# Optimization experiments

Measured on AMD Instinct MI355X. Metric: run time of the kernel, lower is better.

Reference implementation:

```python
import jax, jax.numpy as jnp
import numpy as np
from jax import lax

T, H, I, E, K = 1024, 1024, 512, 16, 4


def setup_inputs() -> dict:
    key = jax.random.key(0)
    k1, k2, k3, k4, k5 = jax.random.split(key, 5)
    hidden_states = jax.random.normal(k1, (T, H), dtype=jnp.float32)
    top_k_index = jax.random.randint(k2, (T, K), 0, E)
    top_k_weights = jax.random.uniform(k3, (T, K), dtype=jnp.float32)
    gate_up_proj = jax.random.normal(k4, (E, 2 * I, H), dtype=jnp.float32) * 0.02
    down_proj = jax.random.normal(k5, (E, H, I), dtype=jnp.float32) * 0.02
    return {
        "hidden_states": hidden_states,
        "top_k_index": top_k_index,
        "top_k_weights": top_k_weights,
        "gate_up_proj": gate_up_proj,
        "down_proj": down_proj,
    }


def reference(hidden_states, top_k_index, top_k_weights, gate_up_proj, down_proj):
    num_experts = gate_up_proj.shape[0]
    # combine[t, e] = sum_k top_k_weights[t, k] * [top_k_index[t, k] == e]
    # Expert output is linear in the routing weight, so summing weights over
    # duplicate (token, expert) hits matches the original index_add_ exactly.
    one_hot = jax.nn.one_hot(top_k_index, num_experts, dtype=hidden_states.dtype)  # [T, K, E]
    combine = jnp.einsum("tke,tk->te", one_hot, top_k_weights)  # [T, E]

    def expert_step(acc, xs):
        w_gu, w_d, c = xs  # [2I, H], [H, I], [T]
        gu = hidden_states @ w_gu.T          # [T, 2I]
        gate, up = jnp.split(gu, 2, axis=-1)
        h = jax.nn.silu(gate) * up            # [T, I]
        out = h @ w_d.T                       # [T, H]
        return acc + out * c[:, None], None

    final, _ = lax.scan(
        expert_step,
        jnp.zeros_like(hidden_states),
        (gate_up_proj, down_proj, combine.T),
    )
    return final
```

## Files before the change

kernel.cpp:

```cpp
#include <hip/hip_runtime.h>
#include <hip/hip_bf16.h>
#include <cstdint>
#include <cstddef>

#define T_TOK 1024
#define HDIM  1024
#define IDIM  512
#define NEXP  16
#define TOPK  4
#define CAP   1024

typedef __bf16 bf16;
typedef __attribute__((ext_vector_type(8))) __bf16 bf16x8;
typedef __attribute__((ext_vector_type(4))) __bf16 bf16x4;
typedef __attribute__((ext_vector_type(4))) float f32x4;

__device__ __forceinline__ void lds_load16(void* lds_dst, const void* g_src) {
  __builtin_amdgcn_global_load_lds(
      (__attribute__((address_space(1))) unsigned int*)(void*)(g_src),
      (__attribute__((address_space(3))) unsigned int*)(lds_dst),
      16, 0, 0);
}

__device__ __forceinline__ bf16x4 cvt4(float4 a) {
  bf16x4 o;
  o[0] = (bf16)a.x; o[1] = (bf16)a.y; o[2] = (bf16)a.z; o[3] = (bf16)a.w;
  return o;
}
__device__ __forceinline__ bf16x8 pack2(float4 a, float4 b) {
  bf16x8 o;
  o[0] = (bf16)a.x; o[1] = (bf16)a.y; o[2] = (bf16)a.z; o[3] = (bf16)a.w;
  o[4] = (bf16)b.x; o[5] = (bf16)b.y; o[6] = (bf16)b.z; o[7] = (bf16)b.w;
  return o;
}


#define CVT_BLOCKS (T_TOK * HDIM / 4 / 256)

__global__ void prep_kernel(const float* __restrict__ hid_f, bf16* __restrict__ hid_b,
                            const int* __restrict__ idx, const float* __restrict__ w,
                            int* __restrict__ etk, float* __restrict__ ew,
                            int* __restrict__ cntpad) {
  __shared__ int cnt;
  const int b = blockIdx.x;
  const int tid = threadIdx.x;
  if (b < CVT_BLOCKS) {
    int i = b * 256 + tid;
    float4 v = ((const float4*)hid_f)[i];
    ((bf16x4*)hid_b)[i] = cvt4(v);
    if (b == 0)
      ((bf16x4*)(hid_b + (size_t)T_TOK * HDIM))[tid] = cvt4(make_float4(0.f, 0.f, 0.f, 0.f));
    return;
  }
  const int e = b - CVT_BLOCKS;
  if (tid == 0) cnt = 0;
  __syncthreads();
  for (int j = tid; j < T_TOK * TOPK; j += blockDim.x) {
    if (idx[j] == e) {
      int slot = atomicAdd(&cnt, 1);
      if (slot < CAP) { etk[e * CAP + slot] = j; ew[e * CAP + slot] = w[j]; }
    }
  }
  __syncthreads();
  int c = cnt < CAP ? cnt : CAP;
  int p = (c + 63) & ~63;
  for (int j = c + tid; j < p; j += blockDim.x) {
    etk[e * CAP + j] = (T_TOK << 2);
    ew[e * CAP + j] = 0.f;
  }
  if (tid == 0) cntpad[e] = p;
}


__global__ __launch_bounds__(256, 3) void gemm1_kernel(
    const bf16* __restrict__ hid,
    const float* __restrict__ gup,
    const int* __restrict__ etk, const float* __restrict__ ew,
    const int* __restrict__ cntpad,
    bf16* __restrict__ hsc) {
  __shared__ __align__(16) bf16 As[2][64 * 128];
  __shared__ __align__(16) bf16 BgS[2][16 * 128];
  __shared__ __align__(16) bf16 BuS[2][16 * 128];
  const int e  = blockIdx.y;
  const int z  = blockIdx.z;
  const int trips = cntpad[e] >> 6;
  const int n0 = blockIdx.x * 16;
  const int ebase = e * CAP;
  const int tid = threadIdx.x, lane = tid & 63, wid = tid >> 6;
  const int wm = wid * 16;
  const int lcol = lane & 15, lquad = lane >> 4;
  const int arow0 = tid >> 4;
  const int swzA  = (((tid & 15) ^ (arow0 & 7)) * 8);
  const int br = tid >> 4;
  const int bc = (tid & 15) * 8;
  const int physB = ((tid & 15) ^ (br & 7)) * 8;
  const float* gBg = gup + (size_t)e * (2 * IDIM) * HDIM + (size_t)(n0 + br) * HDIM + bc;
  const float* gBu = gBg + (size_t)IDIM * HDIM;

  for (int m = z; m < trips; m += 2) {
    const int mb = ebase + m * 64;
    const bf16* gA[4];
#pragma unroll
    for (int i = 0; i < 4; ++i) {
      int t = etk[mb + arow0 + 16 * i] >> 2;
      gA[i] = hid + (size_t)t * HDIM + swzA;
    }
    float wgt[4];
#pragma unroll
    for (int rr = 0; rr < 4; ++rr) wgt[rr] = ew[mb + wm + lquad * 4 + rr];

    f32x4 aG = f32x4{0.f, 0.f, 0.f, 0.f};
    f32x4 aU = f32x4{0.f, 0.f, 0.f, 0.f};

#pragma unroll
    for (int i = 0; i < 4; ++i) lds_load16(&As[0][tid * 8 + i * 2048], gA[i]);
    {
      float4 g0 = *(const float4*)(gBg), g1 = *(const float4*)(gBg + 4);
      float4 u0 = *(const float4*)(gBu), u1 = *(const float4*)(gBu + 4);
      *(bf16x8*)&BgS[0][br * 128 + physB] = pack2(g0, g1);
      *(bf16x8*)&BuS[0][br * 128 + physB] = pack2(u0, u1);
    }
#pragma unroll 2
    for (int k = 0; k < 8; ++k) {
      const int cur = k & 1, nxt = cur ^ 1;
      __syncthreads();
      float4 g0, g1, u0, u1;
      if (k < 7) {
        const int ko = (k + 1) * 128;
#pragma unroll
        for (int i = 0; i < 4; ++i) lds_load16(&As[nxt][tid * 8 + i * 2048], gA[i] + ko);
        g0 = *(const float4*)(gBg + ko); g1 = *(const float4*)(gBg + ko + 4);
        u0 = *(const float4*)(gBu + ko); u1 = *(const float4*)(gBu + ko + 4);
      }
#pragma unroll
      for (int ks = 0; ks < 4; ++ks) {
        const int lch = ks * 4 + lquad;
        const int ar = wm + lcol;
        bf16x8 af = *(const bf16x8*)&As[cur][ar * 128 + ((lch ^ (ar & 7)) * 8)];
        bf16x8 bg = *(const bf16x8*)&BgS[cur][lcol * 128 + ((lch ^ (lcol & 7)) * 8)];
        bf16x8 bu = *(const bf16x8*)&BuS[cur][lcol * 128 + ((lch ^ (lcol & 7)) * 8)];
        aG = __builtin_amdgcn_mfma_f32_16x16x32_bf16(af, bg, aG, 0, 0, 0);
        aU = __builtin_amdgcn_mfma_f32_16x16x32_bf16(af, bu, aU, 0, 0, 0);
      }
      if (k < 7) {
        *(bf16x8*)&BgS[nxt][br * 128 + physB] = pack2(g0, g1);
        *(bf16x8*)&BuS[nxt][br * 128 + physB] = pack2(u0, u1);
      }
    }
#pragma unroll
    for (int rr = 0; rr < 4; ++rr) {
      const int erow = m * 64 + wm + lquad * 4 + rr;
      float g = aG[rr], u = aU[rr];
      float s = g / (1.f + __expf(-g));
      hsc[(size_t)(ebase + erow) * IDIM + n0 + lcol] = (bf16)(s * u * wgt[rr]);
    }
  }
}


__global__ __launch_bounds__(256, 3) void gemm2_kernel(
    const bf16* __restrict__ hsc,
    const float* __restrict__ down,
    const int* __restrict__ etk, const int* __restrict__ cntpad,
    float* __restrict__ slabs) {
  __shared__ __align__(16) bf16 As[2][64 * 128];
  __shared__ __align__(16) bf16 Bs[2][32 * 128];
  const int e  = blockIdx.y;
  const int z  = blockIdx.z;
  const int trips = cntpad[e] >> 6;
  const int n0 = blockIdx.x * 32;
  const int ebase = e * CAP;
  const int tid = threadIdx.x, lane = tid & 63, wid = tid >> 6;
  const int wm = wid * 16;
  const int lcol = lane & 15, lquad = lane >> 4;
  const int arow0 = tid >> 4;
  const int swzA  = (((tid & 15) ^ (arow0 & 7)) * 8);
  const int btr = tid >> 3;
  const int bc  = (tid & 7) * 16;
  const int cb0 = (tid & 7) * 2;
  const int physB0 = (cb0 ^ (btr & 7)) * 8;
  const int physB1 = ((cb0 + 1) ^ (btr & 7)) * 8;
  const float* gB = down + (size_t)e * HDIM * IDIM + (size_t)(n0 + btr) * IDIM + bc;

  for (int m = z; m < trips; m += 2) {
    const int mb = ebase + m * 64;
    const bf16* gA[4];
#pragma unroll
    for (int i = 0; i < 4; ++i)
      gA[i] = hsc + (size_t)(mb + arow0 + 16 * i) * IDIM + swzA;
    int tks[4];
#pragma unroll
    for (int rr = 0; rr < 4; ++rr) tks[rr] = etk[mb + wm + lquad * 4 + rr];

    f32x4 acc0 = f32x4{0.f, 0.f, 0.f, 0.f};
    f32x4 acc1 = f32x4{0.f, 0.f, 0.f, 0.f};

#pragma unroll
    for (int i = 0; i < 4; ++i) lds_load16(&As[0][tid * 8 + i * 2048], gA[i]);
    {
      float4 v0 = *(const float4*)(gB),     v1 = *(const float4*)(gB + 4);
      float4 v2 = *(const float4*)(gB + 8), v3 = *(const float4*)(gB + 12);
      *(bf16x8*)&Bs[0][btr * 128 + physB0] = pack2(v0, v1);
      *(bf16x8*)&Bs[0][btr * 128 + physB1] = pack2(v2, v3);
    }
#pragma unroll 2
    for (int k = 0; k < 4; ++k) {
      const int cur = k & 1, nxt = cur ^ 1;
      __syncthreads();
      float4 v0, v1, v2, v3;
      if (k < 3) {
        const int ko = (k + 1) * 128;
#pragma unroll
        for (int i = 0; i < 4; ++i) lds_load16(&As[nxt][tid * 8 + i * 2048], gA[i] + ko);
        v0 = *(const float4*)(gB + ko);     v1 = *(const float4*)(gB + ko + 4);
        v2 = *(const float4*)(gB + ko + 8); v3 = *(const float4*)(gB + ko + 12);
      }
#pragma unroll
      for (int ks = 0; ks < 4; ++ks) {
        const int lch = ks * 4 + lquad;
        const int ar = wm + lcol;
        bf16x8 af = *(const bf16x8*)&As[cur][ar * 128 + ((lch ^ (ar & 7)) * 8)];
        const int br0 = lcol, br1 = 16 + lcol;
        bf16x8 b0 = *(const bf16x8*)&Bs[cur][br0 * 128 + ((lch ^ (br0 & 7)) * 8)];
        bf16x8 b1 = *(const bf16x8*)&Bs[cur][br1 * 128 + ((lch ^ (br1 & 7)) * 8)];
        acc0 = __builtin_amdgcn_mfma_f32_16x16x32_bf16(af, b0, acc0, 0, 0, 0);
        acc1 = __builtin_amdgcn_mfma_f32_16x16x32_bf16(af, b1, acc1, 0, 0, 0);
      }
      if (k < 3) {
        *(bf16x8*)&Bs[nxt][btr * 128 + physB0] = pack2(v0, v1);
        *(bf16x8*)&Bs[nxt][btr * 128 + physB1] = pack2(v2, v3);
      }
    }
#pragma unroll
    for (int rr = 0; rr < 4; ++rr) {
      const int tok = tks[rr] >> 2, kslot = tks[rr] & 3;
      float* orow = slabs + ((size_t)kslot * (T_TOK + 1) + tok) * HDIM + n0;
      orow[lcol]      = acc0[rr];
      orow[16 + lcol] = acc1[rr];
    }
  }
}


__global__ void reduce_kernel(const float* __restrict__ slabs, float* __restrict__ out) {
  const size_t stride = (size_t)(T_TOK + 1) * HDIM;
  int i = blockIdx.x * blockDim.x + threadIdx.x;
  float4 a = ((const float4*)slabs)[i];
  float4 b = ((const float4*)(slabs + stride))[i];
  float4 c = ((const float4*)(slabs + 2 * stride))[i];
  float4 d = ((const float4*)(slabs + 3 * stride))[i];
  float4 o;
  o.x = a.x + b.x + c.x + d.x;
  o.y = a.y + b.y + c.y + d.y;
  o.z = a.z + b.z + c.z + d.z;
  o.w = a.w + b.w + c.w + d.w;
  ((float4*)out)[i] = o;
}


extern "C" void kernel_launch(void* const* d_in, const int* in_sizes, int n_in,
                              void* d_out, int out_size, void* d_ws, size_t ws_size,
                              hipStream_t stream) {
  const float* hid_f  = (const float*)d_in[0];
  const int*   idx    = (const int*)d_in[1];
  const float* tw     = (const float*)d_in[2];
  const float* gup_f  = (const float*)d_in[3];
  const float* down_f = (const float*)d_in[4];
  float* out = (float*)d_out;

  uint8_t* ws = (uint8_t*)d_ws;
  size_t off = 0;
  bf16* hid_b = (bf16*)(ws + off);   off += (size_t)(T_TOK + 1) * HDIM * 2;
  int*  etk   = (int*)(ws + off);    off += (size_t)NEXP * CAP * 4;
  float* ewt  = (float*)(ws + off);  off += (size_t)NEXP * CAP * 4;
  int* cntpad = (int*)(ws + off);    off += 256;
  bf16* hsc   = (bf16*)(ws + off);   off += (size_t)NEXP * CAP * IDIM * 2;
  float* slabs = (float*)(ws + off);

  prep_kernel<<<dim3(CVT_BLOCKS + NEXP), dim3(256), 0, stream>>>(
      hid_f, hid_b, idx, tw, etk, ewt, cntpad);
  gemm1_kernel<<<dim3(IDIM / 16, NEXP, 2), dim3(256), 0, stream>>>(
      hid_b, gup_f, etk, ewt, cntpad, hsc);
  gemm2_kernel<<<dim3(HDIM / 32, NEXP, 2), dim3(256), 0, stream>>>(
      hsc, down_f, etk, cntpad, slabs);
  reduce_kernel<<<dim3(T_TOK * HDIM / 4 / 256), dim3(256), 0, stream>>>(slabs, out);
}
```

Baseline: 207.4 us.

## Split LDS K-tiles into 64-wide halves and drop z-split of token tiles

Both expert GEMM kernels now store each 128-wide K tile as two 64-column sub-tiles with an 8-chunk XOR swizzle, which changes how global loads map to threads (coalescing per 128B row segment). The z-dimension split of token tiles is removed, so each block handles every M tile of its expert and column slice. The grid is halved and launch_bounds occupancy drops from 3 to 2. This cuts repeated fp32 weight loads per column slice and may improve global access patterns, but it lowers parallelism and occupancy.

```diff
diff --git a/kernel.cpp b/kernel.cpp
--- a/kernel.cpp
+++ b/kernel.cpp
@@ -72,39 +72,36 @@
 }
 
 
-__global__ __launch_bounds__(256, 3) void gemm1_kernel(
+__global__ __launch_bounds__(256, 2) void gemm1_kernel(
     const bf16* __restrict__ hid,
     const float* __restrict__ gup,
     const int* __restrict__ etk, const float* __restrict__ ew,
     const int* __restrict__ cntpad,
     bf16* __restrict__ hsc) {
-  __shared__ __align__(16) bf16 As[2][64 * 128];
-  __shared__ __align__(16) bf16 BgS[2][16 * 128];
-  __shared__ __align__(16) bf16 BuS[2][16 * 128];
+  __shared__ __align__(16) bf16 As[2][2][64 * 64];
+  __shared__ __align__(16) bf16 BgS[2][2][16 * 64];
+  __shared__ __align__(16) bf16 BuS[2][2][16 * 64];
   const int e  = blockIdx.y;
-  const int z  = blockIdx.z;
   const int trips = cntpad[e] >> 6;
   const int n0 = blockIdx.x * 16;
   const int ebase = e * CAP;
   const int tid = threadIdx.x, lane = tid & 63, wid = tid >> 6;
   const int wm = wid * 16;
   const int lcol = lane & 15, lquad = lane >> 4;
-  const int arow0 = tid >> 4;
-  const int swzA  = (((tid & 15) ^ (arow0 & 7)) * 8);
+  const int srow = tid >> 3;
+  const int swz  = ((tid & 7) ^ (srow & 7)) * 8;
   const int br = tid >> 4;
-  const int bc = (tid & 15) * 8;
-  const int physB = ((tid & 15) ^ (br & 7)) * 8;
+  const int bc = (tid & 15) * 4;
+  const int wb = (((bc >> 3) ^ (br & 7)) * 8) + (bc & 7);
   const float* gBg = gup + (size_t)e * (2 * IDIM) * HDIM + (size_t)(n0 + br) * HDIM + bc;
   const float* gBu = gBg + (size_t)IDIM * HDIM;
 
-  for (int m = z; m < trips; m += 2) {
+  for (int m = 0; m < trips; ++m) {
     const int mb = ebase + m * 64;
-    const bf16* gA[4];
-#pragma unroll
-    for (int i = 0; i < 4; ++i) {
-      int t = etk[mb + arow0 + 16 * i] >> 2;
-      gA[i] = hid + (size_t)t * HDIM + swzA;
-    }
+    const int t0 = etk[mb + srow] >> 2;
+    const int t1 = etk[mb + srow + 32] >> 2;
+    const bf16* gA0 = hid + (size_t)t0 * HDIM + swz;
+    const bf16* gA1 = hid + (size_t)t1 * HDIM + swz;
     float wgt[4];
 #pragma unroll
     for (int rr = 0; rr < 4; ++rr) wgt[rr] = ew[mb + wm + lquad * 4 + rr];
@@ -113,38 +110,46 @@
     f32x4 aU = f32x4{0.f, 0.f, 0.f, 0.f};
 
 #pragma unroll
-    for (int i = 0; i < 4; ++i) lds_load16(&As[0][tid * 8 + i * 2048], gA[i]);
-    {
-      float4 g0 = *(const float4*)(gBg), g1 = *(const float4*)(gBg + 4);
-      float4 u0 = *(const float4*)(gBu), u1 = *(const float4*)(gBu + 4);
-      *(bf16x8*)&BgS[0][br * 128 + physB] = pack2(g0, g1);
-      *(bf16x8*)&BuS[0][br * 128 + physB] = pack2(u0, u1);
+    for (int s = 0; s < 2; ++s) {
+      lds_load16(&As[0][s][tid * 8],        gA0 + s * 64);
+      lds_load16(&As[0][s][tid * 8 + 2048], gA1 + s * 64);
+      float4 vg = *(const float4*)(gBg + s * 64);
+      float4 vu = *(const float4*)(gBu + s * 64);
+      *(bf16x4*)&BgS[0][s][br * 64 + wb] = cvt4(vg);
+      *(bf16x4*)&BuS[0][s][br * 64 + wb] = cvt4(vu);
     }
 #pragma unroll 2
     for (int k = 0; k < 8; ++k) {
       const int cur = k & 1, nxt = cur ^ 1;
       __syncthreads();
-      float4 g0, g1, u0, u1;
+      float4 g[2], u[2];
       if (k < 7) {
         const int ko = (k + 1) * 128;
 #pragma unroll
-        for (int i = 0; i < 4; ++i) lds_load16(&As[nxt][tid * 8 + i * 2048], gA[i] + ko);
-        g0 = *(const float4*)(gBg + ko); g1 = *(const float4*)(gBg + ko + 4);
-        u0 = *(const float4*)(gBu + ko); u1 = *(const float4*)(gBu + ko + 4);
+        for (int s = 0; s < 2; ++s) {
+          lds_load16(&As[nxt][s][tid * 8],        gA0 + ko + s * 64);
+          lds_load16(&As[nxt][s][tid * 8 + 2048], gA1 + ko + s * 64);
+          g[s] = *(const float4*)(gBg + ko + s * 64);
+          u[s] = *(const float4*)(gBu + ko + s * 64);
+        }
       }
 #pragma unroll
       for (int ks = 0; ks < 4; ++ks) {
-        const int lch = ks * 4 + lquad;
+        const int sub = ks >> 1;
+        const int lch = (ks & 1) * 4 + lquad;
         const int ar = wm + lcol;
-        bf16x8 af = *(const bf16x8*)&As[cur][ar * 128 + ((lch ^ (ar & 7)) * 8)];
-        bf16x8 bg = *(const bf16x8*)&BgS[cur][lcol * 128 + ((lch ^ (lcol & 7)) * 8)];
-        bf16x8 bu = *(const bf16x8*)&BuS[cur][lcol * 128 + ((lch ^ (lcol & 7)) * 8)];
+        bf16x8 af = *(const bf16x8*)&As[cur][sub][ar * 64 + ((lch ^ (ar & 7)) * 8)];
+        bf16x8 bg = *(const bf16x8*)&BgS[cur][sub][lcol * 64 + ((lch ^ (lcol & 7)) * 8)];
+        bf16x8 bu = *(const bf16x8*)&BuS[cur][sub][lcol * 64 + ((lch ^ (lcol & 7)) * 8)];
         aG = __builtin_amdgcn_mfma_f32_16x16x32_bf16(af, bg, aG, 0, 0, 0);
         aU = __builtin_amdgcn_mfma_f32_16x16x32_bf16(af, bu, aU, 0, 0, 0);
       }
       if (k < 7) {
-        *(bf16x8*)&BgS[nxt][br * 128 + physB] = pack2(g0, g1);
-        *(bf16x8*)&BuS[nxt][br * 128 + physB] = pack2(u0, u1);
+#pragma unroll
+        for (int s = 0; s < 2; ++s) {
+          *(bf16x4*)&BgS[nxt][s][br * 64 + wb] = cvt4(g[s]);
+          *(bf16x4*)&BuS[nxt][s][br * 64 + wb] = cvt4(u[s]);
+        }
       }
     }
 #pragma unroll
@@ -158,77 +163,76 @@
 }
 
 
-__global__ __launch_bounds__(256, 3) void gemm2_kernel(
+__global__ __launch_bounds__(256, 2) void gemm2_kernel(
     const bf16* __restrict__ hsc,
     const float* __restrict__ down,
     const int* __restrict__ etk, const int* __restrict__ cntpad,
     float* __restrict__ slabs) {
-  __shared__ __align__(16) bf16 As[2][64 * 128];
-  __shared__ __align__(16) bf16 Bs[2][32 * 128];
+  __shared__ __align__(16) bf16 As[2][2][64 * 64];
+  __shared__ __align__(16) bf16 Bs[2][2][32 * 64];
   const int e  = blockIdx.y;
-  const int z  = blockIdx.z;
   const int trips = cntpad[e] >> 6;
   const int n0 = blockIdx.x * 32;
   const int ebase = e * CAP;
   const int tid = threadIdx.x, lane = tid & 63, wid = tid >> 6;
   const int wm = wid * 16;
   const int lcol = lane & 15, lquad = lane >> 4;
-  const int arow0 = tid >> 4;
-  const int swzA  = (((tid & 15) ^ (arow0 & 7)) * 8);
+  const int srow = tid >> 3;
+  const int swz  = ((tid & 7) ^ (srow & 7)) * 8;
   const int btr = tid >> 3;
-  const int bc  = (tid & 7) * 16;
-  const int cb0 = (tid & 7) * 2;
-  const int physB0 = (cb0 ^ (btr & 7)) * 8;
-  const int physB1 = ((cb0 + 1) ^ (btr & 7)) * 8;
-  const float* gB = down + (size_t)e * HDIM * IDIM + (size_t)(n0 + btr) * IDIM + bc;
-
-  for (int m = z; m < trips; m += 2) {
+  const int c0  = (tid & 7) * 8;
+  const int wbk = ((tid & 7) ^ (btr & 7)) * 8;
+  const float* gB = down + (size_t)e * HDIM * IDIM + (size_t)(n0 + btr) * IDIM + c0;
+
+  for (int m = 0; m < trips; ++m) {
     const int mb = ebase + m * 64;
-    const bf16* gA[4];
-#pragma unroll
-    for (int i = 0; i < 4; ++i)
-      gA[i] = hsc + (size_t)(mb + arow0 + 16 * i) * IDIM + swzA;
     int tks[4];
 #pragma unroll
     for (int rr = 0; rr < 4; ++rr) tks[rr] = etk[mb + wm + lquad * 4 + rr];
+    const bf16* gA = hsc + (size_t)(mb + srow) * IDIM + swz;
 
     f32x4 acc0 = f32x4{0.f, 0.f, 0.f, 0.f};
     f32x4 acc1 = f32x4{0.f, 0.f, 0.f, 0.f};
 
 #pragma unroll
-    for (int i = 0; i < 4; ++i) lds_load16(&As[0][tid * 8 + i * 2048], gA[i]);
-    {
-      float4 v0 = *(const float4*)(gB),     v1 = *(const float4*)(gB + 4);
-      float4 v2 = *(const float4*)(gB + 8), v3 = *(const float4*)(gB + 12);
-      *(bf16x8*)&Bs[0][btr * 128 + physB0] = pack2(v0, v1);
-      *(bf16x8*)&Bs[0][btr * 128 + physB1] = pack2(v2, v3);
+    for (int s = 0; s < 2; ++s) {
+      lds_load16(&As[0][s][tid * 8],        gA + s * 64);
+      lds_load16(&As[0][s][tid * 8 + 2048], gA + s * 64 + (size_t)32 * IDIM);
+      float4 v0 = *(const float4*)(gB + s * 64);
+      float4 v1 = *(const float4*)(gB + s * 64 + 4);
+      *(bf16x8*)&Bs[0][s][btr * 64 + wbk] = pack2(v0, v1);
     }
 #pragma unroll 2
     for (int k = 0; k < 4; ++k) {
       const int cur = k & 1, nxt = cur ^ 1;
       __syncthreads();
-      float4 v0, v1, v2, v3;
+      float4 v0[2], v1[2];
       if (k < 3) {
         const int ko = (k + 1) * 128;
 #pragma unroll
-        for (int i = 0; i < 4; ++i) lds_load16(&As[nxt][tid * 8 + i * 2048], gA[i] + ko);
-        v0 = *(const float4*)(gB + ko);     v1 = *(const float4*)(gB + ko + 4);
-        v2 = *(const float4*)(gB + ko + 8); v3 = *(const float4*)(gB + ko + 12);
+        for (int s = 0; s < 2; ++s) {
+          lds_load16(&As[nxt][s][tid * 8],        gA + ko + s * 64);
+          lds_load16(&As[nxt][s][tid * 8 + 2048], gA + ko + s * 64 + (size_t)32 * IDIM);
+          v0[s] = *(const float4*)(gB + ko + s * 64);
+          v1[s] = *(const float4*)(gB + ko + s * 64 + 4);
+        }
       }
 #pragma unroll
       for (int ks = 0; ks < 4; ++ks) {
-        const int lch = ks * 4 + lquad;
+        const int sub = ks >> 1;
+        const int lch = (ks & 1) * 4 + lquad;
         const int ar = wm + lcol;
-        bf16x8 af = *(const bf16x8*)&As[cur][ar * 128 + ((lch ^ (ar & 7)) * 8)];
+        bf16x8 af = *(const bf16x8*)&As[cur][sub][ar * 64 + ((lch ^ (ar & 7)) * 8)];
         const int br0 = lcol, br1 = 16 + lcol;
-        bf16x8 b0 = *(const bf16x8*)&Bs[cur][br0 * 128 + ((lch ^ (br0 & 7)) * 8)];
-        bf16x8 b1 = *(const bf16x8*)&Bs[cur][br1 * 128 + ((lch ^ (br1 & 7)) * 8)];
+        bf16x8 b0 = *(const bf16x8*)&Bs[cur][sub][br0 * 64 + ((lch ^ (br0 & 7)) * 8)];
+        bf16x8 b1 = *(const bf16x8*)&Bs[cur][sub][br1 * 64 + ((lch ^ (br1 & 7)) * 8)];
         acc0 = __builtin_amdgcn_mfma_f32_16x16x32_bf16(af, b0, acc0, 0, 0, 0);
         acc1 = __builtin_amdgcn_mfma_f32_16x16x32_bf16(af, b1, acc1, 0, 0, 0);
       }
       if (k < 3) {
-        *(bf16x8*)&Bs[nxt][btr * 128 + physB0] = pack2(v0, v1);
-        *(bf16x8*)&Bs[nxt][btr * 128 + physB1] = pack2(v2, v3);
+#pragma unroll
+        for (int s = 0; s < 2; ++s)
+          *(bf16x8*)&Bs[nxt][s][btr * 64 + wbk] = pack2(v0[s], v1[s]);
       }
     }
 #pragma unroll
@@ -279,9 +283,9 @@
 
   prep_kernel<<<dim3(CVT_BLOCKS + NEXP), dim3(256), 0, stream>>>(
       hid_f, hid_b, idx, tw, etk, ewt, cntpad);
-  gemm1_kernel<<<dim3(IDIM / 16, NEXP, 2), dim3(256), 0, stream>>>(
+  gemm1_kernel<<<dim3(IDIM / 16, NEXP), dim3(256), 0, stream>>>(
       hid_b, gup_f, etk, ewt, cntpad, hsc);
-  gemm2_kernel<<<dim3(HDIM / 32, NEXP, 2), dim3(256), 0, stream>>>(
+  gemm2_kernel<<<dim3(HDIM / 32, NEXP), dim3(256), 0, stream>>>(
       hsc, down_f, etk, cntpad, slabs);
   reduce_kernel<<<dim3(T_TOK * HDIM / 4 / 256), dim3(256), 0, stream>>>(slabs, out);
 }
```

New measurement: 216.3 us. +4.3%, slower.
